# Optimization experiments

Hardware: AMD Instinct MI355X
Metric: run time of the kernel (lower is better)

Reference implementation:

```python
import jax, jax.numpy as jnp
import numpy as np

TEMPERATURE = 0.1
N, D = 8192, 1024

def setup_inputs() -> dict:
    key = jax.random.key(0)
    k1, k2 = jax.random.split(key)
    im = jax.random.normal(k1, (N, D), dtype=jnp.float32)
    cap = jax.random.normal(k2, (N, D), dtype=jnp.float32)
    return {"im": im, "cap": cap}

def reference(im, cap):
    # InfoNCE (info_nce package) L2-normalizes query, positive and negatives.
    # Per-sample loop: for image i, positive = cap[i], negatives = cap[j != i].
    # Logits set = sim(im_i, cap_j) for all j, positive at j == i, so
    # loss_i = logsumexp_j(S[i, j] / T) - S[i, i] / T  (CLIP-style CE).
    imn = im / jnp.linalg.norm(im, axis=-1, keepdims=True)
    capn = cap / jnp.linalg.norm(cap, axis=-1, keepdims=True)
    S = jnp.einsum('id,jd->ij', imn, capn) / TEMPERATURE  # [N, N]
    diag = jnp.diagonal(S)
    loss_i2c = jax.nn.logsumexp(S, axis=1) - diag  # image -> caption direction
    loss_c2i = jax.nn.logsumexp(S, axis=0) - diag  # caption -> image direction
    # original averages all 2N per-sample losses
    return 0.5 * (jnp.mean(loss_i2c) + jnp.mean(loss_c2i))
```

## Files before the change

### kernel.cpp

```cpp
#include <hip/hip_runtime.h>
#include <stdint.h>

#define N_ 8192
#define D_ 1024
#define EPILOGUE_SCALE (10.0f / 256.0f)
#define ENC_SCALE 16.0f
#define CHUNK 524288

typedef float f32x4 __attribute__((ext_vector_type(4)));
typedef float f32x16 __attribute__((ext_vector_type(16)));
typedef int i32x4 __attribute__((ext_vector_type(4)));
typedef int i32x8 __attribute__((ext_vector_type(8)));

#define GLD16(gsrc, ldst)                                                    \
  __builtin_amdgcn_global_load_lds(                                          \
      (const __attribute__((address_space(1))) unsigned int*)(gsrc),         \
      (__attribute__((address_space(3))) unsigned int*)(ldst), 16, 0, 0)


__global__ __launch_bounds__(1024) void normalize_k(
    const float* __restrict__ im, const float* __restrict__ cap,
    unsigned int* __restrict__ imn, unsigned int* __restrict__ capn,
    float* __restrict__ diag, float* __restrict__ sums ) {
  __shared__ unsigned int ldsA[16 * 260];
  __shared__ unsigned int ldsB[16 * 260];
  const int til = blockIdx.x;
  const int t = threadIdx.x;
  if (til < 4) ((float4*)sums)[til * 1024 + t] = (float4){0.f, 0.f, 0.f, 0.f};

  const int r = t >> 6, j = t & 63;
  const int row = til * 16 + r;
  const float4* __restrict__ aR = (const float4*)(im + (size_t)row * D_);
  const float4* __restrict__ bR = (const float4*)(cap + (size_t)row * D_);

  float4 a0 = aR[j], a1 = aR[j + 64], a2 = aR[j + 128], a3 = aR[j + 192];
  float4 b0 = bR[j], b1 = bR[j + 64], b2 = bR[j + 128], b3 = bR[j + 192];

  float ssa = a0.x * a0.x + a0.y * a0.y + a0.z * a0.z + a0.w * a0.w
            + a1.x * a1.x + a1.y * a1.y + a1.z * a1.z + a1.w * a1.w
            + a2.x * a2.x + a2.y * a2.y + a2.z * a2.z + a2.w * a2.w
            + a3.x * a3.x + a3.y * a3.y + a3.z * a3.z + a3.w * a3.w;
  float ssb = b0.x * b0.x + b0.y * b0.y + b0.z * b0.z + b0.w * b0.w
            + b1.x * b1.x + b1.y * b1.y + b1.z * b1.z + b1.w * b1.w
            + b2.x * b2.x + b2.y * b2.y + b2.z * b2.z + b2.w * b2.w
            + b3.x * b3.x + b3.y * b3.y + b3.z * b3.z + b3.w * b3.w;
  float dt  = a0.x * b0.x + a0.y * b0.y + a0.z * b0.z + a0.w * b0.w
            + a1.x * b1.x + a1.y * b1.y + a1.z * b1.z + a1.w * b1.w
            + a2.x * b2.x + a2.y * b2.y + a2.z * b2.z + a2.w * b2.w
            + a3.x * b3.x + a3.y * b3.y + a3.z * b3.z + a3.w * b3.w;
#pragma unroll
  for (int o = 1; o < 64; o <<= 1) {
    ssa += __shfl_xor(ssa, o, 64);
    ssb += __shfl_xor(ssb, o, 64);
    dt  += __shfl_xor(dt, o, 64);
  }
  const float ra = rsqrtf(ssa), rb = rsqrtf(ssb);
  if (j == 0) diag[row] = dt * ra * rb * 10.0f;
  const float sa = ra * ENC_SCALE, sb = rb * ENC_SCALE;

#define CVT_ST(av, bv, ofs)                                                  \
  {                                                                          \
    int pa_ = __builtin_amdgcn_cvt_pk_fp8_f32(av.x * sa, av.y * sa, 0, false); \
    pa_ = __builtin_amdgcn_cvt_pk_fp8_f32(av.z * sa, av.w * sa, pa_, true);  \
    int pb_ = __builtin_amdgcn_cvt_pk_fp8_f32(bv.x * sb, bv.y * sb, 0, false); \
    pb_ = __builtin_amdgcn_cvt_pk_fp8_f32(bv.z * sb, bv.w * sb, pb_, true);  \
    ldsA[r * 260 + j + (ofs)] = (unsigned int)pa_;                           \
    ldsB[r * 260 + j + (ofs)] = (unsigned int)pb_;                           \
  }
  CVT_ST(a0, b0, 0)
  CVT_ST(a1, b1, 64)
  CVT_ST(a2, b2, 128)
  CVT_ST(a3, b3, 192)
#undef CVT_ST
  __syncthreads();

  {
    const int q = t >> 4, rp = t & 15;
    const uint4 va = *(const uint4*)&ldsA[rp * 260 + q * 4];
    const uint4 vb = *(const uint4*)&ldsB[rp * 260 + q * 4];
    const int row32 = ((til & 1) << 4) + rp;
    const size_t d = (size_t)(q >> 2) * CHUNK + (size_t)(til >> 1) * 2048
                   + (size_t)((q & 1) << 10)
                   + (size_t)((((q >> 1) & 1) << 5) + row32) * 16;
    *(uint4*)((unsigned char*)imn + d) = va;
    *(uint4*)((unsigned char*)capn + d) = vb;
  }
}

__global__ __launch_bounds__(512, 4) void gemm_lse_k(
    const unsigned char* __restrict__ A,
    const unsigned char* __restrict__ B,
    float* __restrict__ rowsum, float* __restrict__ colsum) {
  __shared__ unsigned char lds[2][24576];
  const int t = threadIdx.x;
  const int w = t >> 6, l = t & 63;
  const int l16 = l * 16;

  const int bid = blockIdx.x + (blockIdx.y << 5);
  const int nid = (bid & 7) * 256 + (bid >> 3);
  const int rowT = ((nid >> 8) << 2) + (nid & 3);
  const int colT = (nid >> 2) & 63;

  const size_t baseA = (size_t)rowT * 16384;
  const size_t baseB = (size_t)colT * 8192;

  const unsigned char* src[3];
  int ldsOff[3];
#pragma unroll
  for (int c = 0; c < 3; ++c) {
    const int o = w * 3072 + c * 1024;
    ldsOff[c] = o;
    src[c] = (o < 16384) ? (A + baseA + o + l16)
                         : (B + baseB + (o - 16384) + l16);
  }

#define STAGE(kc, buf)                                                       \
  {                                                                          \
    const size_t kofs = (size_t)(kc) * CHUNK;                                \
    GLD16(src[0] + kofs, &lds[buf][ldsOff[0]]);                              \
    GLD16(src[1] + kofs, &lds[buf][ldsOff[1]]);                              \
    GLD16(src[2] + kofs, &lds[buf][ldsOff[2]]);                              \
  }

  const int wr = w >> 1, wc = w & 1;

  f32x16 acc[2][2];
#pragma unroll
  for (int m = 0; m < 2; ++m)
#pragma unroll
    for (int n = 0; n < 2; ++n)
#pragma unroll
      for (int r = 0; r < 16; ++r) acc[m][n][r] = 0.f;

#define COMPUTE(buf)                                                         \
  {                                                                          \
    const unsigned char* Lc = &lds[buf][0];                                  \
    i32x8 a_[2], b_[2];                                                      \
    _Pragma("unroll")                                                        \
    for (int m = 0; m < 2; ++m) {                                            \
      i32x4 lo = *(const i32x4*)(Lc + (wr * 2 + m) * 2048 + l16);            \
      i32x4 hi = *(const i32x4*)(Lc + (wr * 2 + m) * 2048 + 1024 + l16);     \
      a_[m] = __builtin_shufflevector(lo, hi, 0, 1, 2, 3, 4, 5, 6, 7);       \
    }                                                                        \
    _Pragma("unroll")                                                        \
    for (int n = 0; n < 2; ++n) {                                            \
      i32x4 lo = *(const i32x4*)(Lc + 16384 + (wc * 2 + n) * 2048 + l16);    \
      i32x4 hi = *(const i32x4*)(Lc + 16384 + (wc * 2 + n) * 2048 + 1024 + l16); \
      b_[n] = __builtin_shufflevector(lo, hi, 0, 1, 2, 3, 4, 5, 6, 7);       \
    }                                                                        \
    _Pragma("unroll")                                                        \
    for (int m = 0; m < 2; ++m)                                              \
      _Pragma("unroll")                                                      \
      for (int n = 0; n < 2; ++n)                                            \
        acc[m][n] = __builtin_amdgcn_mfma_scale_f32_32x32x64_f8f6f4(         \
            a_[m], b_[n], acc[m][n], 0, 0, 0, 0x7F7F7F7F, 0, 0x7F7F7F7F);    \
  }

  STAGE(0, 0)

#pragma unroll 1
  for (int kt = 0; kt < 15; ++kt) {
    STAGE(kt + 1, (kt + 1) & 1)
    asm volatile("s_waitcnt vmcnt(3)" ::: "memory");
    __builtin_amdgcn_s_barrier();
    COMPUTE(kt & 1)
    __builtin_amdgcn_s_barrier();
  }
  asm volatile("s_waitcnt vmcnt(0)" ::: "memory");
  __builtin_amdgcn_s_barrier();
  COMPUTE(1)
#undef COMPUTE
#undef STAGE

#pragma unroll
  for (int m = 0; m < 2; ++m)
#pragma unroll
    for (int n = 0; n < 2; ++n)
#pragma unroll
      for (int r = 0; r < 16; ++r)
        acc[m][n][r] = __expf(acc[m][n][r] * EPILOGUE_SCALE);

  const int rowBase = rowT * 256 + wr * 64;
  const int colBase = colT * 128 + wc * 64;
#pragma unroll
  for (int m = 0; m < 2; ++m) {
    f32x16 s = acc[m][0] + acc[m][1];
#pragma unroll
    for (int r = 0; r < 16; ++r) {
      float v = s[r];
      v += __shfl_xor(v, 1, 64);
      v += __shfl_xor(v, 2, 64);
      v += __shfl_xor(v, 4, 64);
      v += __shfl_xor(v, 8, 64);
      v += __shfl_xor(v, 16, 64);
      if ((l & 31) == 0)
        atomicAdd(&rowsum[rowBase + m * 32 + (r & 3) + 8 * (r >> 2) + 4 * (l >> 5)], v);
    }
  }
#pragma unroll
  for (int n = 0; n < 2; ++n) {
    float v = 0.f;
#pragma unroll
    for (int r = 0; r < 16; ++r) v += acc[0][n][r] + acc[1][n][r];
    v += __shfl_xor(v, 32, 64);
    if (l < 32)
      atomicAdd(&colsum[colBase + n * 32 + l], v);
  }
}

__global__ __launch_bounds__(256) void finalize_k(
    const float* __restrict__ rowsum, const float* __restrict__ colsum,
    const float* __restrict__ diag, float* __restrict__ out) {
  const int t = threadIdx.x;
  float lse = 0.f, dg = 0.f;
  for (int i = t; i < N_; i += 256) {
    lse += __logf(rowsum[i]) + __logf(colsum[i]);
    dg += diag[i];
  }
#pragma unroll
  for (int o = 32; o > 0; o >>= 1) {
    lse += __shfl_down(lse, o, 64);
    dg  += __shfl_down(dg, o, 64);
  }
  __shared__ float red[2][4];
  const int w = t >> 6, l = t & 63;
  if (l == 0) { red[0][w] = lse; red[1][w] = dg; }
  __syncthreads();
  if (t == 0) {
    lse = red[0][0] + red[0][1] + red[0][2] + red[0][3];
    dg  = red[1][0] + red[1][1] + red[1][2] + red[1][3];
    out[0] = 0.5f * lse / (float)N_ - dg / (float)N_;
  }
}

extern "C" void kernel_launch(void* const* d_in, const int* in_sizes, int n_in,
                              void* d_out, int out_size, void* d_ws, size_t ws_size,
                              hipStream_t stream) {
  const float* im = (const float*)d_in[0];
  const float* cap = (const float*)d_in[1];
  float* out = (float*)d_out;
  char* ws = (char*)d_ws;
  unsigned char* imn = (unsigned char*)ws;
  unsigned char* capn = imn + (size_t)N_ * D_;
  float* rowsum = (float*)(ws + 2 * (size_t)N_ * D_);
  float* colsum = rowsum + N_;
  float* diag = colsum + N_;

  normalize_k<<<512, 1024, 0, stream>>>(im, cap, (unsigned int*)imn,
                                        (unsigned int*)capn, diag, rowsum);
  gemm_lse_k<<<dim3(32, 64), 512, 0, stream>>>(imn, capn, rowsum, colsum);
  finalize_k<<<1, 256, 0, stream>>>(rowsum, colsum, diag, out);
}
```

Before: 196.1 us.

## Load B operands directly into registers and shrink LDS to shared A tile

The GEMM block changes from 512 threads with a 256x128 tile, where A and B are both staged through LDS, to 256 threads with a 128x256 tile. Only the shared A rows go through LDS. Each wave now owns a private 64-column B slice that it loads straight from global memory into registers, double-buffered across two register sets. The aim is to cut LDS traffic and LDS footprint and to give each wave more MFMAs per load (4x2 instead of 2x2). The cost is higher register pressure, fewer threads per block, and B loads that each wave must latency-hide on its own.

```diff
diff --git a/kernel.cpp b/kernel.cpp
--- a/kernel.cpp
+++ b/kernel.cpp
@@ -87,69 +87,69 @@
   }
 }
 
-__global__ __launch_bounds__(512, 4) void gemm_lse_k(
+__global__ __launch_bounds__(256, 2) void gemm_lse_k(
     const unsigned char* __restrict__ A,
     const unsigned char* __restrict__ B,
     float* __restrict__ rowsum, float* __restrict__ colsum) {
-  __shared__ unsigned char lds[2][24576];
+  __shared__ unsigned char lds[2][8192];
   const int t = threadIdx.x;
   const int w = t >> 6, l = t & 63;
   const int l16 = l * 16;
 
-  const int bid = blockIdx.x + (blockIdx.y << 5);
+  const int bid = blockIdx.x + (blockIdx.y << 6);
   const int nid = (bid & 7) * 256 + (bid >> 3);
-  const int rowT = ((nid >> 8) << 2) + (nid & 3);
-  const int colT = (nid >> 2) & 63;
-
-  const size_t baseA = (size_t)rowT * 16384;
-  const size_t baseB = (size_t)colT * 8192;
-
-  const unsigned char* src[3];
-  int ldsOff[3];
-#pragma unroll
-  for (int c = 0; c < 3; ++c) {
-    const int o = w * 3072 + c * 1024;
-    ldsOff[c] = o;
-    src[c] = (o < 16384) ? (A + baseA + o + l16)
-                         : (B + baseB + (o - 16384) + l16);
-  }
+  const int rowT = ((nid >> 8) << 3) + (nid & 7);
+  const int colT = (nid >> 3) & 31;
+
+  const size_t baseA = (size_t)rowT * 8192;
+  const size_t baseB = (size_t)colT * 16384;
+
+  const unsigned char* __restrict__ srcA0 = A + baseA + w * 2048 + l16;
+  const unsigned char* __restrict__ srcA1 = srcA0 + 1024;
+  const int ofsA0 = w * 2048, ofsA1 = ofsA0 + 1024;
+
+  const unsigned char* __restrict__ srcB = B + baseB + w * 4096 + l16;
 
 #define STAGE(kc, buf)                                                       \
   {                                                                          \
     const size_t kofs = (size_t)(kc) * CHUNK;                                \
-    GLD16(src[0] + kofs, &lds[buf][ldsOff[0]]);                              \
-    GLD16(src[1] + kofs, &lds[buf][ldsOff[1]]);                              \
-    GLD16(src[2] + kofs, &lds[buf][ldsOff[2]]);                              \
-  }
-
-  const int wr = w >> 1, wc = w & 1;
-
-  f32x16 acc[2][2];
-#pragma unroll
-  for (int m = 0; m < 2; ++m)
+    GLD16(srcA0 + kofs, &lds[buf][ofsA0]);                                   \
+    GLD16(srcA1 + kofs, &lds[buf][ofsA1]);                                   \
+  }
+
+#define BLOAD(dst, kc)                                                       \
+  {                                                                          \
+    const unsigned char* bp = srcB + (size_t)(kc) * CHUNK;                   \
+    dst[0] = *(const i32x4*)(bp);                                            \
+    dst[1] = *(const i32x4*)(bp + 1024);                                     \
+    dst[2] = *(const i32x4*)(bp + 2048);                                     \
+    dst[3] = *(const i32x4*)(bp + 3072);                                     \
+  }
+
+  f32x16 acc[4][2];
+#pragma unroll
+  for (int m = 0; m < 4; ++m)
 #pragma unroll
     for (int n = 0; n < 2; ++n)
 #pragma unroll
       for (int r = 0; r < 16; ++r) acc[m][n][r] = 0.f;
 
-#define COMPUTE(buf)                                                         \
+  i32x4 bb0[4], bb1[4];
+
+#define COMPUTE(buf, bset)                                                   \
   {                                                                          \
     const unsigned char* Lc = &lds[buf][0];                                  \
-    i32x8 a_[2], b_[2];                                                      \
+    i32x8 a_[4], b_[2];                                                      \
     _Pragma("unroll")                                                        \
-    for (int m = 0; m < 2; ++m) {                                            \
-      i32x4 lo = *(const i32x4*)(Lc + (wr * 2 + m) * 2048 + l16);            \
-      i32x4 hi = *(const i32x4*)(Lc + (wr * 2 + m) * 2048 + 1024 + l16);     \
+    for (int m = 0; m < 4; ++m) {                                            \
+      i32x4 lo = *(const i32x4*)(Lc + m * 2048 + l16);                       \
+      i32x4 hi = *(const i32x4*)(Lc + m * 2048 + 1024 + l16);                \
       a_[m] = __builtin_shufflevector(lo, hi, 0, 1, 2, 3, 4, 5, 6, 7);       \
     }                                                                        \
+    b_[0] = __builtin_shufflevector(bset[0], bset[1], 0, 1, 2, 3, 4, 5, 6, 7); \
+    b_[1] = __builtin_shufflevector(bset[2], bset[3], 0, 1, 2, 3, 4, 5, 6, 7); \
     _Pragma("unroll")                                                        \
-    for (int n = 0; n < 2; ++n) {                                            \
-      i32x4 lo = *(const i32x4*)(Lc + 16384 + (wc * 2 + n) * 2048 + l16);    \
-      i32x4 hi = *(const i32x4*)(Lc + 16384 + (wc * 2 + n) * 2048 + 1024 + l16); \
-      b_[n] = __builtin_shufflevector(lo, hi, 0, 1, 2, 3, 4, 5, 6, 7);       \
-    }                                                                        \
-    _Pragma("unroll")                                                        \
-    for (int m = 0; m < 2; ++m)                                              \
+    for (int m = 0; m < 4; ++m)                                              \
       _Pragma("unroll")                                                      \
       for (int n = 0; n < 2; ++n)                                            \
         acc[m][n] = __builtin_amdgcn_mfma_scale_f32_32x32x64_f8f6f4(         \
@@ -157,33 +157,48 @@
   }
 
   STAGE(0, 0)
+  BLOAD(bb0, 0)
 
 #pragma unroll 1
-  for (int kt = 0; kt < 15; ++kt) {
+  for (int kt = 0; kt < 14; kt += 2) {
     STAGE(kt + 1, (kt + 1) & 1)
-    asm volatile("s_waitcnt vmcnt(3)" ::: "memory");
-    __builtin_amdgcn_s_barrier();
-    COMPUTE(kt & 1)
-    __builtin_amdgcn_s_barrier();
-  }
+    BLOAD(bb1, kt + 1)
+    asm volatile("s_waitcnt vmcnt(6)" ::: "memory");
+    __builtin_amdgcn_s_barrier();
+    COMPUTE(kt & 1, bb0)
+    __builtin_amdgcn_s_barrier();
+    STAGE(kt + 2, (kt + 2) & 1)
+    BLOAD(bb0, kt + 2)
+    asm volatile("s_waitcnt vmcnt(6)" ::: "memory");
+    __builtin_amdgcn_s_barrier();
+    COMPUTE((kt + 1) & 1, bb1)
+    __builtin_amdgcn_s_barrier();
+  }
+  STAGE(15, 1)
+  BLOAD(bb1, 15)
+  asm volatile("s_waitcnt vmcnt(6)" ::: "memory");
+  __builtin_amdgcn_s_barrier();
+  COMPUTE(0, bb0)
+  __builtin_amdgcn_s_barrier();
   asm volatile("s_waitcnt vmcnt(0)" ::: "memory");
   __builtin_amdgcn_s_barrier();
-  COMPUTE(1)
+  COMPUTE(1, bb1)
 #undef COMPUTE
+#undef BLOAD
 #undef STAGE
 
 #pragma unroll
-  for (int m = 0; m < 2; ++m)
+  for (int m = 0; m < 4; ++m)
 #pragma unroll
     for (int n = 0; n < 2; ++n)
 #pragma unroll
       for (int r = 0; r < 16; ++r)
         acc[m][n][r] = __expf(acc[m][n][r] * EPILOGUE_SCALE);
 
-  const int rowBase = rowT * 256 + wr * 64;
-  const int colBase = colT * 128 + wc * 64;
-#pragma unroll
-  for (int m = 0; m < 2; ++m) {
+  const int rowBase = rowT * 128;
+  const int colBase = colT * 256 + w * 64;
+#pragma unroll
+  for (int m = 0; m < 4; ++m) {
     f32x16 s = acc[m][0] + acc[m][1];
 #pragma unroll
     for (int r = 0; r < 16; ++r) {
@@ -201,7 +216,8 @@
   for (int n = 0; n < 2; ++n) {
     float v = 0.f;
 #pragma unroll
-    for (int r = 0; r < 16; ++r) v += acc[0][n][r] + acc[1][n][r];
+    for (int r = 0; r < 16; ++r) v += acc[0][n][r] + acc[1][n][r]
+                                    + acc[2][n][r] + acc[3][n][r];
     v += __shfl_xor(v, 32, 64);
     if (l < 32)
       atomicAdd(&colsum[colBase + n * 32 + l], v);
@@ -248,6 +264,6 @@
 
   normalize_k<<<512, 1024, 0, stream>>>(im, cap, (unsigned int*)imn,
                                         (unsigned int*)capn, diag, rowsum);
-  gemm_lse_k<<<dim3(32, 64), 512, 0, stream>>>(imn, capn, rowsum, colsum);
+  gemm_lse_k<<<dim3(64, 32), 256, 0, stream>>>(imn, capn, rowsum, colsum);
   finalize_k<<<1, 256, 0, stream>>>(rowsum, colsum, diag, out);
 }
```

Measured after the change: 206.1 us. 5.1% more time.
